# Optimization experiments

Hardware: AMD Instinct MI355X
Metric: run time of the kernel (lower is better)

Reference implementation:

```python
import jax, jax.numpy as jnp
import numpy as np

TRUE_CLASS_NUM = 10000   # leaf classes
CLASS_NUM = 16384        # total tree nodes (leaves + internal)
HIDDEN = 512
BATCH = 4096
MAX_DEPTH = 6


def setup_inputs() -> dict:
    key = jax.random.key(0)
    kx, kw, ky = jax.random.split(key, 3)
    x = jax.random.normal(kx, (BATCH, HIDDEN), dtype=jnp.float32)
    y = jax.random.randint(ky, (BATCH,), 0, TRUE_CLASS_NUM, dtype=jnp.int64)
    # linear.weight of nn.Linear(hidden, class_num, bias=False): [class_num, hidden]
    weights = jax.random.normal(kw, (CLASS_NUM, HIDDEN), dtype=jnp.float32) * 0.02
    # new2index: each leaf class j has a path; torch code sums weights[j] plus
    # weights[path[0..len-2]]. We materialize exactly the summed ancestor indices
    # as flat CSR-style (ancestor_idx, segment_id) with variable depth per class.
    rng = np.random.default_rng(0)
    depth = rng.integers(1, MAX_DEPTH + 1, size=TRUE_CLASS_NUM)          # ancestors per class
    ancestor_idx = rng.integers(TRUE_CLASS_NUM, CLASS_NUM, size=int(depth.sum()))
    segment_id = np.repeat(np.arange(TRUE_CLASS_NUM), depth)
    return {
        "x": x,
        "y": y,
        "weights": weights,
        "ancestor_idx": jnp.asarray(ancestor_idx, dtype=jnp.int32),
        "segment_id": jnp.asarray(segment_id, dtype=jnp.int32),
    }


def reference(x, y, weights, ancestor_idx, segment_id):
    # added_weights[j] = weights[j] + sum over ancestors on j's tree path
    anc_sum = jax.ops.segment_sum(weights[ancestor_idx], segment_id,
                                  num_segments=TRUE_CLASS_NUM)  # [T, H]
    added_weights = weights[:TRUE_CLASS_NUM] + anc_sum           # [T, H]
    logits = jnp.einsum('bh,th->bt', x, added_weights)           # [B, T]
    logp = jax.nn.log_softmax(logits, axis=-1)
    loss = -jnp.take_along_axis(logp, y[:, None], axis=1).mean()  # CrossEntropyLoss (mean)
    return (loss, logits)
```

## Files before the change

### kernel.cpp

```cpp
#include <hip/hip_runtime.h>
#include <hip/hip_bf16.h>


typedef __bf16 bf16x8 __attribute__((ext_vector_type(8)));
typedef float f32x4 __attribute__((ext_vector_type(4)));
typedef unsigned short u16x8 __attribute__((ext_vector_type(8)));

#define BATCH 4096
#define HID 512
#define TCLS 10000
#define NPAD 10112
#define NBLK 79

__device__ __forceinline__ unsigned short f2bf(float f) {
    unsigned u = __float_as_uint(f);
    unsigned r = (u + 0x7fffu + ((u >> 16) & 1u)) >> 16;
    return (unsigned short)r;
}

__global__ __launch_bounds__(256) void cvt_x_kernel(const float* __restrict__ x,
                                                    unsigned short* __restrict__ xb, int n) {
    int i = (blockIdx.x * 256 + threadIdx.x) * 4;
    if (i < n) {
        float4 v = *(const float4*)(x + i);
        ushort4 o;
        o.x = f2bf(v.x); o.y = f2bf(v.y); o.z = f2bf(v.z); o.w = f2bf(v.w);
        *(ushort4*)(xb + i) = o;
    }
}

__global__ __launch_bounds__(256) void build_aw_kernel(const float* __restrict__ W,
                                                       const int* __restrict__ anc,
                                                       const int* __restrict__ seg,
                                                       int nnz,
                                                       unsigned short* __restrict__ awb) {
    int j = blockIdx.x;
    int h = threadIdx.x * 2;
    unsigned short* dst = awb + (size_t)j * HID + h;
    if (j >= TCLS) {
        *(ushort2*)dst = make_ushort2(0, 0);
        return;
    }
    int lo = 0, hi = nnz;
    while (lo < hi) { int mid = (lo + hi) >> 1; if (seg[mid] < j) lo = mid + 1; else hi = mid; }
    int start = lo;
    hi = nnz;
    while (lo < hi) { int mid = (lo + hi) >> 1; if (seg[mid] <= j) lo = mid + 1; else hi = mid; }
    int end = lo;
    float2 a = *(const float2*)(W + (size_t)j * HID + h);
    for (int k = start; k < end; k++) {
        float2 w = *(const float2*)(W + (size_t)anc[k] * HID + h);
        a.x += w.x; a.y += w.y;
    }
    ushort2 o; o.x = f2bf(a.x); o.y = f2bf(a.y);
    *(ushort2*)dst = o;
}

#define BM 128
#define BN 128
#define BK 32
__global__ __launch_bounds__(256) void gemm_fused_kernel(const unsigned short* __restrict__ A,
                                                         const unsigned short* __restrict__ B,
                                                         float* __restrict__ C,
                                                         float2* __restrict__ partials) {
    __shared__ __align__(16) unsigned char smem[32 * 132 * 4];
    unsigned short* lds_a = (unsigned short*)smem;
    unsigned short* lds_b = ((unsigned short*)smem) + BM * BK;
    float* ldsc = (float*)smem;
    float2* pm = (float2*)smem;

    const int tid = threadIdx.x;
    const int bm = blockIdx.y * BM;
    const int bn = blockIdx.x * BN;
    const int wave = tid >> 6;
    const int lane = tid & 63;
    const int l15 = lane & 15;
    const int quad = lane >> 4;
    const int wm = (wave >> 1) * 64;
    const int wn = (wave & 1) * 64;

    f32x4 acc[4][4];
#pragma unroll
    for (int i = 0; i < 4; i++)
#pragma unroll
        for (int j = 0; j < 4; j++) acc[i][j] = (f32x4)0.f;

    const int c0 = tid, c1 = tid + 256;
    const unsigned short* a_g0 = A + (size_t)(bm + (c0 >> 2)) * HID + (c0 & 3) * 8;
    const unsigned short* a_g1 = A + (size_t)(bm + (c1 >> 2)) * HID + (c1 & 3) * 8;
    const unsigned short* b_g0 = B + (size_t)(bn + (c0 >> 2)) * HID + (c0 & 3) * 8;
    const unsigned short* b_g1 = B + (size_t)(bn + (c1 >> 2)) * HID + (c1 & 3) * 8;
    unsigned short* a_l0 = &lds_a[c0 * 8];
    unsigned short* a_l1 = &lds_a[c1 * 8];
    unsigned short* b_l0 = &lds_b[c0 * 8];
    unsigned short* b_l1 = &lds_b[c1 * 8];

    u16x8 ra0 = *(const u16x8*)a_g0;
    u16x8 ra1 = *(const u16x8*)a_g1;
    u16x8 rb0 = *(const u16x8*)b_g0;
    u16x8 rb1 = *(const u16x8*)b_g1;

    for (int k0 = 0; k0 < HID; k0 += BK) {
        *(u16x8*)a_l0 = ra0;
        *(u16x8*)a_l1 = ra1;
        *(u16x8*)b_l0 = rb0;
        *(u16x8*)b_l1 = rb1;
        __syncthreads();

        int kn = k0 + BK;
        if (kn < HID) {
            ra0 = *(const u16x8*)(a_g0 + kn);
            ra1 = *(const u16x8*)(a_g1 + kn);
            rb0 = *(const u16x8*)(b_g0 + kn);
            rb1 = *(const u16x8*)(b_g1 + kn);
        }

        bf16x8 af[4], bfr[4];
#pragma unroll
        for (int mt = 0; mt < 4; mt++)
            af[mt] = *(const bf16x8*)&lds_a[(wm + mt * 16 + l15) * BK + quad * 8];
#pragma unroll
        for (int nt = 0; nt < 4; nt++)
            bfr[nt] = *(const bf16x8*)&lds_b[(wn + nt * 16 + l15) * BK + quad * 8];
#pragma unroll
        for (int mt = 0; mt < 4; mt++)
#pragma unroll
            for (int nt = 0; nt < 4; nt++)
                acc[mt][nt] = __builtin_amdgcn_mfma_f32_16x16x32_bf16(af[mt], bfr[nt],
                                                                      acc[mt][nt], 0, 0, 0);
        __syncthreads();
    }

    const int colbase = bn + wn + l15;
#pragma unroll
    for (int mt = 0; mt < 4; mt++) {
#pragma unroll
        for (int r = 0; r < 4; r++) {
            float v[4];
#pragma unroll
            for (int nt = 0; nt < 4; nt++)
                v[nt] = (colbase + nt * 16 < TCLS) ? acc[mt][nt][r] : -1e30f;
            float m = fmaxf(fmaxf(v[0], v[1]), fmaxf(v[2], v[3]));
#pragma unroll
            for (int off = 1; off < 16; off <<= 1)
                m = fmaxf(m, __shfl_xor(m, off, 64));
            float s = __expf(v[0] - m) + __expf(v[1] - m) +
                      __expf(v[2] - m) + __expf(v[3] - m);
#pragma unroll
            for (int off = 1; off < 16; off <<= 1)
                s += __shfl_xor(s, off, 64);
            if (l15 == 0) {
                int rowl = wm + mt * 16 + quad * 4 + r;
                pm[rowl * 2 + (wave & 1)] = make_float2(m, s);
            }
        }
    }
    __syncthreads();
    if (tid < 128) {
        float2 p0 = pm[tid * 2 + 0];
        float2 p1 = pm[tid * 2 + 1];
        float nm = fmaxf(p0.x, p1.x);
        float s = p0.y * __expf(p0.x - nm) + p1.y * __expf(p1.x - nm);
        partials[(size_t)(bm + tid) * NBLK + blockIdx.x] = make_float2(nm, s);
    }
    __syncthreads();

#pragma unroll
    for (int t = 0; t < 4; t++) {
        if ((wave >> 1) == (t >> 1)) {
            int mtbase = (t & 1) * 2;
#pragma unroll
            for (int mi = 0; mi < 2; mi++) {
                int mt = mtbase + mi;
                int rowl = mi * 16 + quad * 4;
#pragma unroll
                for (int nt = 0; nt < 4; nt++)
#pragma unroll
                    for (int r = 0; r < 4; r++)
                        ldsc[(rowl + r) * 132 + wn + nt * 16 + l15] = acc[mt][nt][r];
            }
        }
        __syncthreads();
#pragma unroll
        for (int e = 0; e < 16; e++) {
            int idx = e * 256 + tid;
            int rowl = idx >> 7;
            int col = idx & 127;
            int gc = bn + col;
            if (gc < TCLS)
                C[(size_t)(bm + t * 32 + rowl) * TCLS + gc] = ldsc[rowl * 132 + col];
        }
        __syncthreads();
    }
}

__global__ __launch_bounds__(256) void lse_kernel(const float2* __restrict__ partials,
                                                  const float* __restrict__ logits,
                                                  const int* __restrict__ y,
                                                  float* __restrict__ terms) {
    int row = blockIdx.x * 4 + (threadIdx.x >> 6);
    int lane = threadIdx.x & 63;
    float m = -1e30f, s = 0.f;
    if (lane < NBLK) {
        float2 p = partials[(size_t)row * NBLK + lane];
        m = p.x; s = p.y;
    }
    if (lane + 64 < NBLK) {
        float2 p = partials[(size_t)row * NBLK + lane + 64];
        float nm = fmaxf(m, p.x);
        s = s * __expf(m - nm) + p.y * __expf(p.x - nm);
        m = nm;
    }
#pragma unroll
    for (int off = 1; off < 64; off <<= 1) {
        float om = __shfl_xor(m, off, 64);
        float os = __shfl_xor(s, off, 64);
        float nm = fmaxf(m, om);
        s = s * __expf(m - nm) + os * __expf(om - nm);
        m = nm;
    }
    if (lane == 0)
        terms[row] = m + __logf(s) - logits[(size_t)row * TCLS + y[row]];
}

__global__ __launch_bounds__(256) void reduce_loss_kernel(const float* __restrict__ terms,
                                                          float* __restrict__ out) {
    float s = 0.f;
    for (int i = threadIdx.x; i < BATCH; i += 256) s += terms[i];
#pragma unroll
    for (int off = 32; off > 0; off >>= 1) s += __shfl_down(s, off, 64);
    __shared__ float sh[4];
    if ((threadIdx.x & 63) == 0) sh[threadIdx.x >> 6] = s;
    __syncthreads();
    if (threadIdx.x == 0) out[0] = (sh[0] + sh[1] + sh[2] + sh[3]) * (1.0f / BATCH);
}

extern "C" void kernel_launch(void* const* d_in, const int* in_sizes, int n_in,
                              void* d_out, int out_size, void* d_ws, size_t ws_size,
                              hipStream_t stream) {
    const float* x = (const float*)d_in[0];
    const int* y = (const int*)d_in[1];
    const float* W = (const float*)d_in[2];
    const int* anc = (const int*)d_in[3];
    const int* seg = (const int*)d_in[4];
    int nnz = in_sizes[3];

    unsigned short* xb = (unsigned short*)d_ws;
    unsigned short* awb = xb + (size_t)BATCH * HID;
    float2* partials = (float2*)(awb + (size_t)NPAD * HID);
    float* terms = (float*)(partials + (size_t)BATCH * NBLK);
    float* loss = (float*)d_out;
    float* logits = loss + 1;

    cvt_x_kernel<<<(BATCH * HID) / (256 * 4), 256, 0, stream>>>(x, xb, BATCH * HID);
    build_aw_kernel<<<NPAD, 256, 0, stream>>>(W, anc, seg, nnz, awb);
    dim3 grid(NPAD / BN, BATCH / BM);
    gemm_fused_kernel<<<grid, 256, 0, stream>>>(xb, awb, logits, partials);
    lse_kernel<<<BATCH / 4, 256, 0, stream>>>(partials, logits, y, terms);
    reduce_loss_kernel<<<1, 256, 0, stream>>>(terms, loss);
}
```

Baseline: 335.7 us.

## Precompute segment bounds, remap GEMM blocks per XCD, vectorize logits stores

A new kernel computes per-class start/end offsets from segment_id once, replacing two binary searches per block in the weight-building kernel. That kernel now handles two classes per block with float4 loads. The GEMM grid is flattened and remapped so consecutive block IDs on each XCD share column tiles, which should improve L2 reuse. Logit stores use float4 writes shifted by 3 floats to match the 10000-wide row stride, with scalar fallbacks at the edges. One small extra launch is added, and the store path gets more branches.

```diff
diff --git a/kernel.cpp b/kernel.cpp
--- a/kernel.cpp
+++ b/kernel.cpp
@@ -29,31 +29,37 @@
     }
 }
 
+__global__ __launch_bounds__(256) void bounds_kernel(const int* __restrict__ seg, int nnz,
+                                                     int* __restrict__ start,
+                                                     int* __restrict__ end) {
+    int i = blockIdx.x * 256 + threadIdx.x;
+    if (i >= nnz) return;
+    int s = seg[i];
+    if (i == 0 || seg[i - 1] != s) start[s] = i;
+    if (i == nnz - 1 || seg[i + 1] != s) end[s] = i + 1;
+}
+
 __global__ __launch_bounds__(256) void build_aw_kernel(const float* __restrict__ W,
                                                        const int* __restrict__ anc,
-                                                       const int* __restrict__ seg,
-                                                       int nnz,
+                                                       const int* __restrict__ start,
+                                                       const int* __restrict__ end,
                                                        unsigned short* __restrict__ awb) {
-    int j = blockIdx.x;
-    int h = threadIdx.x * 2;
+    int j = blockIdx.x * 2 + (threadIdx.x >> 7);
+    int h = (threadIdx.x & 127) * 4;
     unsigned short* dst = awb + (size_t)j * HID + h;
     if (j >= TCLS) {
-        *(ushort2*)dst = make_ushort2(0, 0);
+        *(ushort4*)dst = make_ushort4(0, 0, 0, 0);
         return;
     }
-    int lo = 0, hi = nnz;
-    while (lo < hi) { int mid = (lo + hi) >> 1; if (seg[mid] < j) lo = mid + 1; else hi = mid; }
-    int start = lo;
-    hi = nnz;
-    while (lo < hi) { int mid = (lo + hi) >> 1; if (seg[mid] <= j) lo = mid + 1; else hi = mid; }
-    int end = lo;
-    float2 a = *(const float2*)(W + (size_t)j * HID + h);
-    for (int k = start; k < end; k++) {
-        float2 w = *(const float2*)(W + (size_t)anc[k] * HID + h);
-        a.x += w.x; a.y += w.y;
-    }
-    ushort2 o; o.x = f2bf(a.x); o.y = f2bf(a.y);
-    *(ushort2*)dst = o;
+    float4 a = *(const float4*)(W + (size_t)j * HID + h);
+    int st = start[j], en = end[j];
+    for (int k = st; k < en; k++) {
+        float4 w = *(const float4*)(W + (size_t)anc[k] * HID + h);
+        a.x += w.x; a.y += w.y; a.z += w.z; a.w += w.w;
+    }
+    ushort4 o;
+    o.x = f2bf(a.x); o.y = f2bf(a.y); o.z = f2bf(a.z); o.w = f2bf(a.w);
+    *(ushort4*)dst = o;
 }
 
 #define BM 128
@@ -69,9 +75,14 @@
     float* ldsc = (float*)smem;
     float2* pm = (float2*)smem;
 
+    const int cid = blockIdx.x;
+    const int xcd = cid & 7;
+    const int lid = cid >> 3;
+    const int bm = (xcd + 8 * (lid & 3)) * BM;
+    const int cb = lid >> 2;
+    const int bn = cb * BN;
+
     const int tid = threadIdx.x;
-    const int bm = blockIdx.y * BM;
-    const int bn = blockIdx.x * BN;
     const int wave = tid >> 6;
     const int lane = tid & 63;
     const int l15 = lane & 15;
@@ -161,7 +172,7 @@
         float2 p1 = pm[tid * 2 + 1];
         float nm = fmaxf(p0.x, p1.x);
         float s = p0.y * __expf(p0.x - nm) + p1.y * __expf(p1.x - nm);
-        partials[(size_t)(bm + tid) * NBLK + blockIdx.x] = make_float2(nm, s);
+        partials[(size_t)(bm + tid) * NBLK + cb] = make_float2(nm, s);
     }
     __syncthreads();
 
@@ -182,13 +193,29 @@
         }
         __syncthreads();
 #pragma unroll
-        for (int e = 0; e < 16; e++) {
-            int idx = e * 256 + tid;
-            int rowl = idx >> 7;
-            int col = idx & 127;
-            int gc = bn + col;
-            if (gc < TCLS)
-                C[(size_t)(bm + t * 32 + rowl) * TCLS + gc] = ldsc[rowl * 132 + col];
+        for (int i = 0; i < 4; i++) {
+            int idx = i * 256 + tid;
+            int rowl = idx >> 5;
+            int q = idx & 31;
+            float* rowp = C + (size_t)(bm + t * 32 + rowl) * TCLS + bn;
+            const float* lrow = ldsc + rowl * 132;
+            if (q < 31) {
+                int colL = 3 + q * 4;
+                if (bn + colL + 3 < TCLS) {
+                    float4 v = make_float4(lrow[colL], lrow[colL + 1],
+                                           lrow[colL + 2], lrow[colL + 3]);
+                    *(float4*)(rowp + colL) = v;
+                } else {
+#pragma unroll
+                    for (int e = 0; e < 4; e++)
+                        if (bn + colL + e < TCLS) rowp[colL + e] = lrow[colL + e];
+                }
+            } else {
+                const int cl[4] = {0, 1, 2, 127};
+#pragma unroll
+                for (int e = 0; e < 4; e++)
+                    if (bn + cl[e] < TCLS) rowp[cl[e]] = lrow[cl[e]];
+            }
         }
         __syncthreads();
     }
@@ -249,13 +276,15 @@
     unsigned short* awb = xb + (size_t)BATCH * HID;
     float2* partials = (float2*)(awb + (size_t)NPAD * HID);
     float* terms = (float*)(partials + (size_t)BATCH * NBLK);
+    int* start = (int*)(terms + BATCH);
+    int* end = start + TCLS;
     float* loss = (float*)d_out;
     float* logits = loss + 1;
 
     cvt_x_kernel<<<(BATCH * HID) / (256 * 4), 256, 0, stream>>>(x, xb, BATCH * HID);
-    build_aw_kernel<<<NPAD, 256, 0, stream>>>(W, anc, seg, nnz, awb);
-    dim3 grid(NPAD / BN, BATCH / BM);
-    gemm_fused_kernel<<<grid, 256, 0, stream>>>(xb, awb, logits, partials);
+    bounds_kernel<<<(nnz + 255) / 256, 256, 0, stream>>>(seg, nnz, start, end);
+    build_aw_kernel<<<NPAD / 2, 256, 0, stream>>>(W, anc, start, end, awb);
+    gemm_fused_kernel<<<(NPAD / BN) * (BATCH / BM), 256, 0, stream>>>(xb, awb, logits, partials);
     lse_kernel<<<BATCH / 4, 256, 0, stream>>>(partials, logits, y, terms);
     reduce_loss_kernel<<<1, 256, 0, stream>>>(terms, loss);
 }
```

New measurement: 309.9 us. -7.7%, faster.
